# Kernel optimization log

Measured on AMD Instinct MI355X. Metric: run time of the kernel, lower is better.

The kernel has to match this reference:

```python
import jax, jax.numpy as jnp
import numpy as np

IO_EMB = 128; IO_HID = 512; ENC_HID = 1024
B = 256; N_IO = 4; L = 64; T = 32; NPROD = 64; VOCAB = 128


def setup_inputs() -> dict:
    key = jax.random.key(0)
    ks = jax.random.split(key, 16)
    s = 0.02
    return {
        'exs_toks': jax.random.randint(ks[0], (L, B * N_IO), 0, VOCAB),
        'cls_toks': jax.random.randint(ks[1], (L, B * N_IO), 0, VOCAB),
        'E_io': jax.random.normal(ks[2], (VOCAB, IO_EMB)) * s,
        'Wi_f': jax.random.normal(ks[3], (2 * IO_EMB, 4 * IO_HID)) * s,
        'Wh_f': jax.random.normal(ks[4], (IO_HID, 4 * IO_HID)) * s,
        'b_f': jnp.zeros((4 * IO_HID,)),
        'Wi_b': jax.random.normal(ks[5], (2 * IO_EMB, 4 * IO_HID)) * s,
        'Wh_b': jax.random.normal(ks[6], (IO_HID, 4 * IO_HID)) * s,
        'b_b': jnp.zeros((4 * IO_HID,)),
        'W_attn': jax.random.normal(ks[7], (ENC_HID, 2 * IO_HID)) * s,
        'W_comp': jax.random.normal(ks[8], (ENC_HID + 2 * IO_HID, NPROD)) * s,
        'b_comp': jnp.zeros((NPROD,)),
        'v_Wi': jax.random.normal(ks[9], (ENC_HID, 4 * ENC_HID)) * s,
        'v_Wh': jax.random.normal(ks[10], (ENC_HID, 4 * ENC_HID)) * s,
        'v_b': jnp.zeros((4 * ENC_HID,)),
        'field_emb': jax.random.normal(ks[11], (T, ENC_HID)) * s,
        'actions': jax.random.randint(ks[12], (B, T), 0, NPROD),
    }


def _lstm(x, Wi, Wh, b, reverse=False):
    # x: [L, N, D] -> hs [L, N, H], final (h, c)
    H = Wh.shape[0]
    N = x.shape[1]
    def step(carry, xt):
        h, c = carry
        g = xt @ Wi + h @ Wh + b
        i, f, gg, o = jnp.split(g, 4, axis=-1)
        c = jax.nn.sigmoid(f) * c + jax.nn.sigmoid(i) * jnp.tanh(gg)
        h = jax.nn.sigmoid(o) * jnp.tanh(c)
        return (h, c), h
    init = (jnp.zeros((N, H), x.dtype), jnp.zeros((N, H), x.dtype))
    (hT, cT), hs = jax.lax.scan(step, init, x, reverse=reverse)
    return hs, hT, cT


def reference(exs_toks, cls_toks, E_io, Wi_f, Wh_f, b_f, Wi_b, Wh_b, b_b,
              W_attn, W_comp, b_comp, v_Wi, v_Wh, v_b, field_emb, actions):
    # --- encode_io: concat exs/cls embeddings, run biLSTM ---
    x = jnp.concatenate([E_io[exs_toks], E_io[cls_toks]], axis=-1)  # [L, B*N_IO, 2*IO_EMB]
    hs_f, hTf, cTf = _lstm(x, Wi_f, Wh_f, b_f)
    hs_b, hTb, cTb = _lstm(x, Wi_b, Wh_b, b_b, reverse=True)
    ctx_vecs = jnp.concatenate([hs_f, hs_b], -1).reshape(L, B, N_IO, 2 * IO_HID)
    # init decoder state: max over io examples of final biLSTM state
    h0 = jnp.concatenate([hTf, hTb], -1).reshape(B, N_IO, ENC_HID).max(axis=1)
    c0 = jnp.concatenate([cTf, cTb], -1).reshape(B, N_IO, ENC_HID).max(axis=1)

    def dec_step(carry, xs):
        h, c, acc = carry
        x_t, a_t = xs  # field embedding [ENC_HID], action ids [B]
        # Luong attention over io context vecs, per io example, then max-pool
        q = h @ W_attn                               # [B, 2*IO_HID]
        scores = jnp.einsum('lbne,be->lbn', ctx_vecs, q)
        attn = jax.nn.softmax(scores, axis=0)
        ctx = jnp.einsum('lbn,lbne->bne', attn, ctx_vecs).max(axis=1)  # [B, 2*IO_HID]
        # per-node classifier (composite type module): negative log-prob of chosen prod
        logits = jnp.concatenate([h, ctx], -1) @ W_comp + b_comp
        logp = jax.nn.log_softmax(logits, axis=-1)
        acc = acc - logp[jnp.arange(B), a_t]
        # constructor update via v_lstm cell
        g = x_t @ v_Wi + h @ v_Wh + v_b
        i, f, gg, o = jnp.split(g, 4, axis=-1)
        c = jax.nn.sigmoid(f) * c + jax.nn.sigmoid(i) * jnp.tanh(gg)
        h = jax.nn.sigmoid(o) * jnp.tanh(c)
        return (h, c, acc), None

    init = (h0, c0, jnp.zeros((B,), h0.dtype))
    (_, _, total), _ = jax.lax.scan(dec_step, init, (field_emb, actions.T))
    return total  # [B] per-program negative log-likelihood
```

## Files before the change

### kernel.cpp

```cpp
#include <hip/hip_runtime.h>
#include <hip/hip_bf16.h>

typedef __bf16 bf16x8 __attribute__((ext_vector_type(8)));
typedef float  f32x4  __attribute__((ext_vector_type(4)));
typedef float  f32x2  __attribute__((ext_vector_type(2)));
typedef unsigned int u32x4 __attribute__((ext_vector_type(4)));
typedef unsigned short ushort_t;
static_assert(sizeof(bf16x8) == 16, "bf16x8 must be 16B");

#define DEV __device__ __forceinline__

DEV f32x4 mfma16(bf16x8 a, bf16x8 b, f32x4 c) {
    return __builtin_amdgcn_mfma_f32_16x16x32_bf16(a, b, c, 0, 0, 0);
}
DEV f32x4 mfma8(long a, long b, f32x4 c) {
    return __builtin_amdgcn_mfma_f32_16x16x32_fp8_fp8(a, b, c, 0, 0, 0);
}
DEV float sigm(float x)   { return 1.0f / (1.0f + __expf(-x)); }
DEV float tanh_f(float x) { return 2.0f / (1.0f + __expf(-2.0f * x)) - 1.0f; }

DEV void glds16(const __hip_bfloat16* g, __hip_bfloat16* l) {
    __builtin_amdgcn_global_load_lds(
        (const __attribute__((address_space(1))) unsigned int*)g,
        (__attribute__((address_space(3))) unsigned int*)l, 16, 0, 0);
}

DEV unsigned char f32_to_fp8(float v) {
    int p = __builtin_amdgcn_cvt_pk_fp8_f32(v, v, 0, false);
    return (unsigned char)(p & 0xFF);
}

DEV int i4get(const int4& v, int r) {
    return r == 0 ? v.x : r == 1 ? v.y : r == 2 ? v.z : v.w;
}

__global__ __launch_bounds__(128) void kdetect(const unsigned int* __restrict__ raw,
                                               int* __restrict__ mode) {
    __shared__ int cnt;
    if (threadIdx.x == 0) cnt = 0;
    __syncthreads();
    unsigned int w = raw[threadIdx.x];
    unsigned short lo = (unsigned short)(w & 0xFFFFu);
    unsigned int f32bits = ((unsigned int)lo) << 16;
    float v;
    __builtin_memcpy(&v, &f32bits, 4);
    float a = fabsf(v);
    if (a >= 1e-4f && a <= 1.0f) atomicAdd(&cnt, 1);
    __syncthreads();
    if (threadIdx.x == 0) *mode = (cnt >= 64) ? 1 : 0;
}

struct CvtArgs {
    const void* src[6];
    void* dst[6];
    int n[6];
    int bf16out[6];
};
__global__ __launch_bounds__(256) void kcvt_all(CvtArgs a, const int* __restrict__ mode) {
    int seg = blockIdx.y;
    int i = blockIdx.x * 256 + threadIdx.x;
    if (i >= a.n[seg]) return;
    int m = *mode;
    if (a.bf16out[seg]) {
        __hip_bfloat16* d = (__hip_bfloat16*)a.dst[seg];
        d[i] = m ? ((const __hip_bfloat16*)a.src[seg])[i]
                 : __float2bfloat16(((const float*)a.src[seg])[i]);
    } else {
        float* d = (float*)a.dst[seg];
        d[i] = m ? __bfloat162float(((const __hip_bfloat16*)a.src[seg])[i])
                 : ((const float*)a.src[seg])[i];
    }
}

struct TransArgs {
    const void* src[8];
    __hip_bfloat16* dst[8];
    int R[8];
    int C[8];
};
__global__ __launch_bounds__(256) void ktrans_all(TransArgs a, const int* __restrict__ mode) {
    __shared__ float tile[64][65];
    int id = blockIdx.z;
    int R = a.R[id], C = a.C[id];
    int c0 = blockIdx.x * 64, r0 = blockIdx.y * 64;
    if (c0 >= C || r0 >= R) return;
    const void* src = a.src[id];
    __hip_bfloat16* out = a.dst[id];
    int tx = threadIdx.x & 63, ty = threadIdx.x >> 6;
    int m = *mode;
#pragma unroll
    for (int i = ty; i < 64; i += 4) {
        size_t ix = (size_t)(r0 + i) * C + (c0 + tx);
        tile[i][tx] = m ? __bfloat162float(((const __hip_bfloat16*)src)[ix])
                        : ((const float*)src)[ix];
    }
    __syncthreads();
#pragma unroll
    for (int i = ty; i < 64; i += 4)
        out[(size_t)(c0 + i) * R + (r0 + tx)] = __float2bfloat16(tile[tx][i]);
}

__global__ __launch_bounds__(256) void kprep_all(
    const __hip_bfloat16* __restrict__ E,
    const __hip_bfloat16* __restrict__ WiT,
    const float* __restrict__ bF,
    const float* __restrict__ bB,
    float* __restrict__ G,
    const __hip_bfloat16* __restrict__ fe,
    const __hip_bfloat16* __restrict__ vWiT,
    const float* __restrict__ vb,
    float* __restrict__ VX)
{
    int lane = threadIdx.x & 63, wid = threadIdx.x >> 6;
    int r16 = lane & 15, quad = lane >> 4;

    if (blockIdx.x < 256) {
        int bid = blockIdx.x;
        int dh = bid >> 6;
        int dir = dh >> 1, half = dh & 1;
        int m0 = ((bid >> 5) & 1) * 64;
        int n0 = (bid & 31) * 64;
        int wrow = wid >> 1, wcol = wid & 1;

        f32x4 acc[2][2] = {};
        const __hip_bfloat16* Ap = E + (size_t)(m0 + wrow * 32 + r16) * 128 + quad * 8;
        const __hip_bfloat16* Bp = WiT + (size_t)dir * 2048 * 256
                                 + (size_t)(n0 + wcol * 32 + r16) * 256 + half * 128 + quad * 8;
#pragma unroll
        for (int kb = 0; kb < 128; kb += 32) {
            bf16x8 a0 = *(const bf16x8*)(Ap + kb);
            bf16x8 a1 = *(const bf16x8*)(Ap + 16 * 128 + kb);
            bf16x8 b0 = *(const bf16x8*)(Bp + kb);
            bf16x8 b1 = *(const bf16x8*)(Bp + 16 * 256 + kb);
            acc[0][0] = mfma16(a0, b0, acc[0][0]);
            acc[0][1] = mfma16(a0, b1, acc[0][1]);
            acc[1][0] = mfma16(a1, b0, acc[1][0]);
            acc[1][1] = mfma16(a1, b1, acc[1][1]);
        }
        const float* bias = dir ? bB : bF;
        float* Gt = G + (size_t)dh * 128 * 2048;
#pragma unroll
        for (int rt = 0; rt < 2; rt++)
#pragma unroll
            for (int ct = 0; ct < 2; ct++)
#pragma unroll
                for (int r = 0; r < 4; r++) {
                    int mm = m0 + wrow * 32 + rt * 16 + quad * 4 + r;
                    int j = n0 + wcol * 32 + ct * 16 + r16;
                    float v = acc[rt][ct][r];
                    if (half == 0) v += bias[j];
                    int g = j >> 9, u = j & 511;
                    Gt[((size_t)mm * 512 + u) * 4 + g] = v;
                }
    } else {
        int n0 = (blockIdx.x - 256) * 128;
        f32x4 acc[2][2] = {};
        const __hip_bfloat16* Ap = fe + (size_t)r16 * 1024 + quad * 8;
        const __hip_bfloat16* Bp = vWiT + (size_t)(n0 + wid * 32 + r16) * 1024 + quad * 8;
        for (int kb = 0; kb < 1024; kb += 32) {
            bf16x8 a0 = *(const bf16x8*)(Ap + kb);
            bf16x8 a1 = *(const bf16x8*)(Ap + 16 * 1024 + kb);
            bf16x8 b0 = *(const bf16x8*)(Bp + kb);
            bf16x8 b1 = *(const bf16x8*)(Bp + 16 * 1024 + kb);
            acc[0][0] = mfma16(a0, b0, acc[0][0]);
            acc[0][1] = mfma16(a0, b1, acc[0][1]);
            acc[1][0] = mfma16(a1, b0, acc[1][0]);
            acc[1][1] = mfma16(a1, b1, acc[1][1]);
        }
#pragma unroll
        for (int rt = 0; rt < 2; rt++)
#pragma unroll
            for (int ct = 0; ct < 2; ct++)
#pragma unroll
                for (int r = 0; r < 4; r++) {
                    int m = rt * 16 + quad * 4 + r;
                    int j = n0 + wid * 32 + ct * 16 + r16;
                    VX[(size_t)m * 4096 + j] = acc[rt][ct][r] + vb[j];
                }
    }
}

__global__ __launch_bounds__(256, 2) void kenc_step(
    int t,
    const __hip_bfloat16* __restrict__ WhT,
    const float* __restrict__ Gtab,
    const int* __restrict__ exs,
    const int* __restrict__ cls,
    const __hip_bfloat16* __restrict__ h_in,
    __hip_bfloat16* __restrict__ h_out,
    float* __restrict__ c_st,
    unsigned char* __restrict__ ctx8)
{
    __shared__ __align__(16) __hip_bfloat16 sA[3][64 * 64];
    __shared__ __align__(16) __hip_bfloat16 sB[3][128 * 64];

    int bid = blockIdx.x;
    int dir = bid >> 8;
    int mt  = (bid >> 4) & 15;
    int us  = bid & 15;
    int l = dir ? (63 - t) : t;
    int m0 = mt * 64, u0 = us * 32;

    int lane = threadIdx.x & 63, w = threadIdx.x >> 6;
    int wm = w >> 1, wu = w & 1;
    int r16 = lane & 15, quad = lane >> 4;
    int srow = lane >> 3;
    int scol = ((lane & 7) ^ srow) * 8;

    const __hip_bfloat16* Ab = h_in + (size_t)dir * 1024 * 512;
    const __hip_bfloat16* Bb = WhT + (size_t)dir * 2048 * 512;

    int u = u0 + wu * 16 + r16;
    int mbase = m0 + wm * 32;
    size_t cbase = (size_t)dir * 1024 * 512;
    const float* GeT = Gtab + (size_t)(dir * 2) * 128 * 2048;
    const float* GcT = GeT + 128 * 2048;

    int4 tE0 = *(const int4*)&exs[l * 1024 + mbase + quad * 4];
    int4 tE1 = *(const int4*)&exs[l * 1024 + mbase + 16 + quad * 4];
    int4 tC0 = *(const int4*)&cls[l * 1024 + mbase + quad * 4];
    int4 tC1 = *(const int4*)&cls[l * 1024 + mbase + 16 + quad * 4];

    f32x4 acc[4][2] = {};
    f32x4 geP[2][4], gcP[2][4];
    float cP[2][4];

    auto stage = [&](int buf, int it) {
        int kb = it * 64;
#pragma unroll
        for (int c = 0; c < 2; c++) {
            int r8 = (w * 2 + c) * 8;
            glds16(Ab + (size_t)(m0 + r8 + srow) * 512 + kb + scol,
                   &sA[buf][r8 * 64]);
        }
#pragma unroll
        for (int c = 0; c < 4; c++) {
            int rl = (w * 4 + c) * 8;
            int rr = rl + srow;
            int g = rr >> 5, j = rr & 31;
            glds16(Bb + (size_t)(g * 512 + u0 + j) * 512 + kb + scol,
                   &sB[buf][rl * 64]);
        }
    };

    stage(0, 0);
    stage(1, 1);

    const int sw = r16 & 7;
    const int NIT = 8;
#pragma unroll
    for (int it = 0; it < NIT; it++) {
        if (it < NIT - 1)
            asm volatile("s_waitcnt vmcnt(6) lgkmcnt(0)" ::: "memory");
        else
            asm volatile("s_waitcnt vmcnt(24) lgkmcnt(0)" ::: "memory");
        __builtin_amdgcn_s_barrier();
        if (it + 2 < NIT) {
            stage((it + 2) % 3, it + 2);
        } else if (it == NIT - 2) {
#pragma unroll
            for (int mi = 0; mi < 2; mi++)
#pragma unroll
                for (int r = 0; r < 4; r++) {
                    int vE = i4get(mi ? tE1 : tE0, r);
                    int vC = i4get(mi ? tC1 : tC0, r);
                    geP[mi][r] = *(const f32x4*)&GeT[((size_t)vE * 512 + u) * 4];
                    gcP[mi][r] = *(const f32x4*)&GcT[((size_t)vC * 512 + u) * 4];
                    int m = mbase + mi * 16 + quad * 4 + r;
                    cP[mi][r] = c_st[cbase + (size_t)m * 512 + u];
                }
        }
        const int buf = it % 3;
#pragma unroll
        for (int k32 = 0; k32 < 64; k32 += 32) {
            int co = (((k32 >> 3) + quad) ^ sw) * 8;
            bf16x8 a[2], bf[4];
#pragma unroll
            for (int mi = 0; mi < 2; mi++)
                a[mi] = *(const bf16x8*)&sA[buf][(wm * 32 + mi * 16 + r16) * 64 + co];
#pragma unroll
            for (int g = 0; g < 4; g++)
                bf[g] = *(const bf16x8*)&sB[buf][(g * 32 + wu * 16 + r16) * 64 + co];
#pragma unroll
            for (int g = 0; g < 4; g++)
#pragma unroll
                for (int mi = 0; mi < 2; mi++)
                    acc[g][mi] = mfma16(a[mi], bf[g], acc[g][mi]);
        }
    }

#pragma unroll
    for (int mi = 0; mi < 2; mi++)
#pragma unroll
        for (int r = 0; r < 4; r++) {
            int m = mbase + mi * 16 + quad * 4 + r;
            f32x4 ge = geP[mi][r];
            f32x4 gc = gcP[mi][r];
            float gi = acc[0][mi][r] + ge[0] + gc[0];
            float gf = acc[1][mi][r] + ge[1] + gc[1];
            float gg = acc[2][mi][r] + ge[2] + gc[2];
            float go = acc[3][mi][r] + ge[3] + gc[3];
            size_t cix = cbase + (size_t)m * 512 + u;
            float cn = sigm(gf) * cP[mi][r] + sigm(gi) * tanh_f(gg);
            c_st[cix] = cn;
            float hn = sigm(go) * tanh_f(cn);
            h_out[cix] = __float2bfloat16(hn);
            ctx8[(((size_t)l * 256 + (m >> 2)) * 4 + (m & 3)) * 1024 + dir * 512 + u]
                = f32_to_fp8(hn * 16.0f);
        }
}

__global__ __launch_bounds__(256) void ktrans8_init(
    const unsigned char* __restrict__ ctx8,
    unsigned char* __restrict__ ctxT8,
    const __hip_bfloat16* __restrict__ hf,
    const float* __restrict__ cf,
    __hip_bfloat16* __restrict__ h0,
    float* __restrict__ c0)
{
    __shared__ unsigned int tile[64][17];
    int bx = blockIdx.x;
    int tid = threadIdx.x;
    if (bx < 16384) {
        int b4n = bx & 1023;
        int e0 = (bx >> 10) * 64;
#pragma unroll
        for (int pass = 0; pass < 4; pass++) {
            int idx = pass * 256 + tid;
            int l = idx >> 4, c = idx & 15;
            tile[l][c] = *(const unsigned int*)(ctx8 + (size_t)l * (1024 * 1024)
                                                + (size_t)b4n * 1024 + e0 + c * 4);
        }
        __syncthreads();
        const unsigned char* tb = (const unsigned char*)tile;
#pragma unroll
        for (int pass = 0; pass < 4; pass++) {
            int idx = pass * 256 + tid;
            int e = idx >> 4, c = idx & 15;
            unsigned int v = 0;
#pragma unroll
            for (int j = 0; j < 4; j++) {
                unsigned int byte = tb[(size_t)(c * 4 + j) * 68 + e];
                v |= byte << (8 * j);
            }
            *(unsigned int*)(ctxT8 + ((size_t)b4n * 1024 + e0 + e) * 64 + c * 4) = v;
        }
    } else {
        int idx = (bx - 16384) * 256 + tid;
        int b = idx >> 10, e = idx & 1023;
        int dir = e >> 9, u = e & 511;
        const __hip_bfloat16* hs = hf + (size_t)dir * 1024 * 512;
        const float* cs = cf + (size_t)dir * 1024 * 512;
        float hv = -3.4e38f, cv = -3.4e38f;
#pragma unroll
        for (int n = 0; n < 4; n++) {
            size_t ix = (size_t)(b * 4 + n) * 512 + u;
            hv = fmaxf(hv, __bfloat162float(hs[ix]));
            cv = fmaxf(cv, cs[ix]);
        }
        h0[idx] = __float2bfloat16(hv);
        c0[idx] = cv;
    }
}

__global__ __launch_bounds__(256, 2) void kdec_gemm(
    int t,
    const __hip_bfloat16* __restrict__ vWhT,
    const __hip_bfloat16* __restrict__ WattnT,
    const float* __restrict__ VX,
    const __hip_bfloat16* __restrict__ h_in,
    __hip_bfloat16* __restrict__ h_out,
    float* __restrict__ c_st,
    float* __restrict__ qout)
{
    __shared__ __align__(16) __hip_bfloat16 sA[3][64 * 64];
    __shared__ __align__(16) __hip_bfloat16 sB[3][128 * 64];

    int bid = blockIdx.x;
    int lane = threadIdx.x & 63, w = threadIdx.x >> 6;
    int wm = w >> 1, wu = w & 1;
    int r16 = lane & 15, quad = lane >> 4;
    int srow = lane >> 3;
    int scol = ((lane & 7) ^ srow) * 8;
    const int NIT = 16;
    const int sw = r16 & 7;

    bool cellp = bid < 128;
    int b2 = cellp ? bid : bid - 128;
    int m0 = (b2 >> 5) * 64;
    int n0 = (b2 & 31) * 32;
    int u = n0 + wu * 16 + r16;
    int mbase = m0 + wm * 32;

    if (cellp) {
        f32x4 acc[4][2] = {};
        float vxP[4], cP[2][4];
        const float* vx = VX + (size_t)t * 4096;
        auto stage = [&](int buf, int it) {
            int kb = it * 64;
#pragma unroll
            for (int c = 0; c < 2; c++) {
                int r8 = (w * 2 + c) * 8;
                glds16(h_in + (size_t)(m0 + r8 + srow) * 1024 + kb + scol,
                       &sA[buf][r8 * 64]);
            }
#pragma unroll
            for (int c = 0; c < 4; c++) {
                int rl = (w * 4 + c) * 8;
                int rr = rl + srow;
                int g = rr >> 5, j = rr & 31;
                glds16(vWhT + (size_t)(g * 1024 + n0 + j) * 1024 + kb + scol,
                       &sB[buf][rl * 64]);
            }
        };
        stage(0, 0);
        stage(1, 1);
#pragma unroll
        for (int it = 0; it < NIT; it++) {
            if (it < NIT - 1)
                asm volatile("s_waitcnt vmcnt(6) lgkmcnt(0)" ::: "memory");
            else
                asm volatile("s_waitcnt vmcnt(12) lgkmcnt(0)" ::: "memory");
            __builtin_amdgcn_s_barrier();
            if (it + 2 < NIT) {
                stage((it + 2) % 3, it + 2);
            } else if (it == NIT - 2) {
                vxP[0] = vx[u];
                vxP[1] = vx[1024 + u];
                vxP[2] = vx[2048 + u];
                vxP[3] = vx[3072 + u];
#pragma unroll
                for (int mi = 0; mi < 2; mi++)
#pragma unroll
                    for (int r = 0; r < 4; r++) {
                        int m = mbase + mi * 16 + quad * 4 + r;
                        cP[mi][r] = c_st[(size_t)m * 1024 + u];
                    }
            }
            const int buf = it % 3;
#pragma unroll
            for (int k32 = 0; k32 < 64; k32 += 32) {
                int co = (((k32 >> 3) + quad) ^ sw) * 8;
                bf16x8 a[2], bf[4];
#pragma unroll
                for (int mi = 0; mi < 2; mi++)
                    a[mi] = *(const bf16x8*)&sA[buf][(wm * 32 + mi * 16 + r16) * 64 + co];
#pragma unroll
                for (int g = 0; g < 4; g++)
                    bf[g] = *(const bf16x8*)&sB[buf][(g * 32 + wu * 16 + r16) * 64 + co];
#pragma unroll
                for (int g = 0; g < 4; g++)
#pragma unroll
                    for (int mi = 0; mi < 2; mi++)
                        acc[g][mi] = mfma16(a[mi], bf[g], acc[g][mi]);
            }
        }
#pragma unroll
        for (int mi = 0; mi < 2; mi++)
#pragma unroll
            for (int r = 0; r < 4; r++) {
                int m = mbase + mi * 16 + quad * 4 + r;
                float gi = acc[0][mi][r] + vxP[0];
                float gf = acc[1][mi][r] + vxP[1];
                float gg = acc[2][mi][r] + vxP[2];
                float go = acc[3][mi][r] + vxP[3];
                size_t cix = (size_t)m * 1024 + u;
                float cn = sigm(gf) * cP[mi][r] + sigm(gi) * tanh_f(gg);
                c_st[cix] = cn;
                h_out[cix] = __float2bfloat16(sigm(go) * tanh_f(cn));
            }
    } else {
        f32x4 acc[2] = {};
        auto stage = [&](int buf, int it) {
            int kb = it * 64;
#pragma unroll
            for (int c = 0; c < 2; c++) {
                int r8 = (w * 2 + c) * 8;
                glds16(h_in + (size_t)(m0 + r8 + srow) * 1024 + kb + scol,
                       &sA[buf][r8 * 64]);
            }
            {
                int rl = w * 8;
                glds16(WattnT + (size_t)(n0 + rl + srow) * 1024 + kb + scol,
                       &sB[buf][rl * 64]);
            }
        };
        stage(0, 0);
        stage(1, 1);
#pragma unroll
        for (int it = 0; it < NIT; it++) {
            if (it < NIT - 1)
                asm volatile("s_waitcnt vmcnt(3) lgkmcnt(0)" ::: "memory");
            else
                asm volatile("s_waitcnt vmcnt(0) lgkmcnt(0)" ::: "memory");
            __builtin_amdgcn_s_barrier();
            if (it + 2 < NIT) stage((it + 2) % 3, it + 2);
            const int buf = it % 3;
#pragma unroll
            for (int k32 = 0; k32 < 64; k32 += 32) {
                int co = (((k32 >> 3) + quad) ^ sw) * 8;
                bf16x8 a[2];
#pragma unroll
                for (int mi = 0; mi < 2; mi++)
                    a[mi] = *(const bf16x8*)&sA[buf][(wm * 32 + mi * 16 + r16) * 64 + co];
                bf16x8 bf = *(const bf16x8*)&sB[buf][(wu * 16 + r16) * 64 + co];
#pragma unroll
                for (int mi = 0; mi < 2; mi++)
                    acc[mi] = mfma16(a[mi], bf, acc[mi]);
            }
        }
        int n = n0 + wu * 16 + r16;
#pragma unroll
        for (int mi = 0; mi < 2; mi++)
#pragma unroll
            for (int r = 0; r < 4; r++) {
                int m = mbase + mi * 16 + quad * 4 + r;
                qout[(size_t)m * 1024 + n] = acc[mi][r];
            }
    }
}

__global__ __launch_bounds__(512, 2) void kattn_mfma(
    const float* __restrict__ qall,
    const unsigned char* __restrict__ ctx8,
    const unsigned char* __restrict__ ctxT8,
    const __hip_bfloat16* __restrict__ hAll,
    const __hip_bfloat16* __restrict__ WcT,
    const float* __restrict__ bcomp,
    const int* __restrict__ actions,
    float* __restrict__ nllT)
{
    __shared__ __align__(16) char smem[75520];
    unsigned char* sQ8   = (unsigned char*)smem;
    float*         sS    = (float*)(smem + 33024);
    unsigned char* sP    = (unsigned char*)(smem + 66304);
    ushort_t*      sPool = (ushort_t*)smem;
    float*         slg   = (float*)(smem + 66304);

    int b = blockIdx.x;
    int tid = threadIdx.x;
    int lane = tid & 63, w = tid >> 6;
    int r16 = lane & 15, quad = lane >> 4;
    const size_t LSTR = 1024 * 1024;

    for (int i = 0; i < 64; i++) {
        int idx = i * 512 + tid;
        int t = idx >> 10, e = idx & 1023;
        float v = qall[((size_t)t * 256 + b) * 1024 + e] * 0.25f;
        sQ8[t * 1032 + e] = f32_to_fp8(v);
    }
    __syncthreads();

    {
        int n = w >> 1, lh = w & 1;
        int l0 = lh * 32;
        f32x4 c[2][2] = {};
        const unsigned char* cbase = ctx8 + (size_t)(b * 4 + n) * 1024;
        for (int k0 = 0; k0 < 1024; k0 += 32) {
            long a[2], bv[2];
#pragma unroll
            for (int mt = 0; mt < 2; mt++)
                __builtin_memcpy(&a[mt], &sQ8[(mt * 16 + r16) * 1032 + k0 + quad * 8], 8);
#pragma unroll
            for (int lt = 0; lt < 2; lt++)
                bv[lt] = *(const long*)(cbase + (size_t)(l0 + lt * 16 + r16) * LSTR
                                        + k0 + quad * 8);
#pragma unroll
            for (int mt = 0; mt < 2; mt++)
#pragma unroll
                for (int lt = 0; lt < 2; lt++)
                    c[mt][lt] = mfma8(a[mt], bv[lt], c[mt][lt]);
        }
#pragma unroll
        for (int mt = 0; mt < 2; mt++)
#pragma unroll
            for (int lt = 0; lt < 2; lt++)
#pragma unroll
                for (int r = 0; r < 4; r++)
                    sS[(n * 32 + mt * 16 + quad * 4 + r) * 65 + l0 + lt * 16 + r16]
                        = c[mt][lt][r];
    }
    __syncthreads();

    if (tid < 128) {
        int n = tid >> 5, t = tid & 31;
        const float* row = &sS[(n * 32 + t) * 65];
        float sum = 0.f;
        for (int l = 0; l < 64; l++)
            sum += __expf(fminf(row[l] * 0.25f, 60.f));
        float inv = 16.0f / sum;
        unsigned char* pr = &sP[(n * 32 + t) * 72];
        for (int l = 0; l < 64; l++)
            pr[l] = f32_to_fp8(__expf(fminf(row[l] * 0.25f, 60.f)) * inv);
    }
    __syncthreads();

    {
        int e0 = w * 128;
        f32x4 pool[2][8];
#pragma unroll
        for (int mt = 0; mt < 2; mt++)
#pragma unroll
            for (int et = 0; et < 8; et++)
#pragma unroll
                for (int r = 0; r < 4; r++) pool[mt][et][r] = -3.4e38f;

        for (int n = 0; n < 4; n++) {
            f32x4 c[2][8] = {};
            const unsigned char* tbase = ctxT8 + (size_t)(b * 4 + n) * 1024 * 64;
#pragma unroll
            for (int k0 = 0; k0 < 64; k0 += 32) {
                long a[2];
#pragma unroll
                for (int mt = 0; mt < 2; mt++)
                    __builtin_memcpy(&a[mt], &sP[(n * 32 + mt * 16 + r16) * 72 + k0 + quad * 8], 8);
#pragma unroll
                for (int et = 0; et < 8; et++) {
                    long bv = *(const long*)(tbase + (size_t)(e0 + et * 16 + r16) * 64
                                             + k0 + quad * 8);
#pragma unroll
                    for (int mt = 0; mt < 2; mt++)
                        c[mt][et] = mfma8(a[mt], bv, c[mt][et]);
                }
            }
#pragma unroll
            for (int mt = 0; mt < 2; mt++)
#pragma unroll
                for (int et = 0; et < 8; et++)
#pragma unroll
                    for (int r = 0; r < 4; r++)
                        pool[mt][et][r] = fmaxf(pool[mt][et][r], c[mt][et][r] * (1.0f / 256.0f));
        }
        __syncthreads();
#pragma unroll
        for (int mt = 0; mt < 2; mt++)
#pragma unroll
            for (int et = 0; et < 8; et++)
#pragma unroll
                for (int r = 0; r < 4; r++) {
                    int t = mt * 16 + quad * 4 + r;
                    int e = e0 + et * 16 + r16;
                    __hip_bfloat16 hb = __float2bfloat16(pool[mt][et][r]);
                    sPool[t * 1032 + e] = *(ushort_t*)&hb;
                }
    }
    __syncthreads();

    {
        int mt = w & 1, pt = w >> 1;
        f32x4 c = {};
        const __hip_bfloat16* hrow = hAll + ((size_t)(mt * 16 + r16) * 256 + b) * 1024;
        const __hip_bfloat16* wrow = WcT + (size_t)(pt * 16 + r16) * 2048;
        for (int k0 = 0; k0 < 2048; k0 += 32) {
            bf16x8 a;
            if (k0 < 1024)
                a = *(const bf16x8*)(hrow + k0 + quad * 8);
            else
                a = *(const bf16x8*)&sPool[(mt * 16 + r16) * 1032 + (k0 - 1024) + quad * 8];
            bf16x8 bv = *(const bf16x8*)(wrow + k0 + quad * 8);
            c = mfma16(a, bv, c);
        }
        __syncthreads();
#pragma unroll
        for (int r = 0; r < 4; r++) {
            int t = mt * 16 + quad * 4 + r;
            int p = pt * 16 + r16;
            slg[t * 68 + p] = c[r] + bcomp[p];
        }
    }
    __syncthreads();

    if (tid < 32) {
        int t = tid;
        const float* row = &slg[t * 68];
        float m = -3.4e38f;
        for (int p = 0; p < 64; p++) m = fmaxf(m, row[p]);
        float se = 0.f;
        for (int p = 0; p < 64; p++) se += __expf(row[p] - m);
        int a = actions[b * 32 + t];
        nllT[t * 256 + b] = m + __logf(se) - row[a];
    }
}

__global__ void kfinal(const float* __restrict__ nllT, void* __restrict__ out,
                       const int* __restrict__ mode) {
    int i = threadIdx.x;
    float s = 0.f;
#pragma unroll
    for (int t = 0; t < 32; t++) s += nllT[t * 256 + i];
    if (*mode) ((__hip_bfloat16*)out)[i] = __float2bfloat16(s);
    else       ((float*)out)[i] = s;
}

extern "C" void kernel_launch(void* const* d_in, const int* in_sizes, int n_in,
                              void* d_out, int out_size, void* d_ws, size_t ws_size,
                              hipStream_t stream) {
    const int* exs = (const int*)d_in[0];
    const int* cls = (const int*)d_in[1];
    const void* E_raw     = d_in[2];
    const void* WiF_raw   = d_in[3];
    const void* WhF_raw   = d_in[4];
    const void* bF_raw    = d_in[5];
    const void* WiB_raw   = d_in[6];
    const void* WhB_raw   = d_in[7];
    const void* bB_raw    = d_in[8];
    const void* Wattn_raw = d_in[9];
    const void* Wcomp_raw = d_in[10];
    const void* bcomp_raw = d_in[11];
    const void* vWi_raw   = d_in[12];
    const void* vWh_raw   = d_in[13];
    const void* vb_raw    = d_in[14];
    const void* fe_raw    = d_in[15];
    const int* actions = (const int*)d_in[16];
    (void)in_sizes; (void)n_in; (void)out_size; (void)ws_size;

    char* w = (char*)d_ws;
    size_t off = 0;
    auto take = [&](size_t bytes) -> char* {
        char* p = w + off;
        off = (off + bytes + 255) & ~(size_t)255;
        return p;
    };
    __hip_bfloat16* WhT    = (__hip_bfloat16*)take(2ull * 2048 * 512 * 2);
    __hip_bfloat16* WiT    = (__hip_bfloat16*)take(2ull * 2048 * 256 * 2);
    __hip_bfloat16* vWhT   = (__hip_bfloat16*)take(4096ull * 1024 * 2);
    __hip_bfloat16* vWiT   = (__hip_bfloat16*)take(4096ull * 1024 * 2);
    __hip_bfloat16* WattnT = (__hip_bfloat16*)take(1024ull * 1024 * 2);
    __hip_bfloat16* WcT    = (__hip_bfloat16*)take(64ull * 2048 * 2);
    __hip_bfloat16* Ebf    = (__hip_bfloat16*)take(128ull * 128 * 2);
    __hip_bfloat16* febf   = (__hip_bfloat16*)take(32ull * 1024 * 2);
    float* bFf   = (float*)take(2048 * 4);
    float* bBf   = (float*)take(2048 * 4);
    float* bcf   = (float*)take(64 * 4);
    float* vbf   = (float*)take(4096 * 4);
    float* Gtab  = (float*)take(4ull * 128 * 2048 * 4);
    float* VX    = (float*)take(32ull * 4096 * 4);
    __hip_bfloat16* hEnc = (__hip_bfloat16*)take(2ull * 2 * 1024 * 512 * 2);
    float* cEnc = (float*)take(2ull * 1024 * 512 * 4);
    __hip_bfloat16* hAll = (__hip_bfloat16*)take(33ull * 256 * 1024 * 2);
    float* cDec = (float*)take(256ull * 1024 * 4);
    float* qall = (float*)take(32ull * 256 * 1024 * 4);
    float* nllT = (float*)take(32ull * 256 * 4);
    int*   mode = (int*)take(256);
    unsigned char* ctx8  = (unsigned char*)take(64ull * 1024 * 1024);
    unsigned char* ctxT8 = (unsigned char*)take(64ull * 1024 * 1024);

    (void)hipMemsetAsync(hEnc, 0, 2ull * 1024 * 512 * 2, stream);
    (void)hipMemsetAsync(cEnc, 0, 2ull * 1024 * 512 * 4, stream);

    kdetect<<<1, 128, 0, stream>>>((const unsigned int*)E_raw, mode);

    {
        CvtArgs ca;
        ca.src[0] = E_raw;     ca.dst[0] = Ebf;  ca.n[0] = 128 * 128;  ca.bf16out[0] = 1;
        ca.src[1] = fe_raw;    ca.dst[1] = febf; ca.n[1] = 32 * 1024;  ca.bf16out[1] = 1;
        ca.src[2] = bF_raw;    ca.dst[2] = bFf;  ca.n[2] = 2048;       ca.bf16out[2] = 0;
        ca.src[3] = bB_raw;    ca.dst[3] = bBf;  ca.n[3] = 2048;       ca.bf16out[3] = 0;
        ca.src[4] = bcomp_raw; ca.dst[4] = bcf;  ca.n[4] = 64;         ca.bf16out[4] = 0;
        ca.src[5] = vb_raw;    ca.dst[5] = vbf;  ca.n[5] = 4096;       ca.bf16out[5] = 0;
        kcvt_all<<<dim3(128, 6), 256, 0, stream>>>(ca, mode);
    }

    {
        TransArgs ta;
        ta.src[0] = WhF_raw;   ta.dst[0] = WhT;              ta.R[0] = 512;  ta.C[0] = 2048;
        ta.src[1] = WhB_raw;   ta.dst[1] = WhT + 2048 * 512; ta.R[1] = 512;  ta.C[1] = 2048;
        ta.src[2] = WiF_raw;   ta.dst[2] = WiT;              ta.R[2] = 256;  ta.C[2] = 2048;
        ta.src[3] = WiB_raw;   ta.dst[3] = WiT + 2048 * 256; ta.R[3] = 256;  ta.C[3] = 2048;
        ta.src[4] = vWh_raw;   ta.dst[4] = vWhT;             ta.R[4] = 1024; ta.C[4] = 4096;
        ta.src[5] = vWi_raw;   ta.dst[5] = vWiT;             ta.R[5] = 1024; ta.C[5] = 4096;
        ta.src[6] = Wattn_raw; ta.dst[6] = WattnT;           ta.R[6] = 1024; ta.C[6] = 1024;
        ta.src[7] = Wcomp_raw; ta.dst[7] = WcT;              ta.R[7] = 2048; ta.C[7] = 64;
        ktrans_all<<<dim3(64, 32, 8), 256, 0, stream>>>(ta, mode);
    }

    kprep_all<<<288, 256, 0, stream>>>(Ebf, WiT, bFf, bBf, Gtab, febf, vWiT, vbf, VX);

    const size_t HB = 2ull * 1024 * 512;
    for (int t = 0; t < 64; t++) {
        kenc_step<<<512, 256, 0, stream>>>(t, WhT, Gtab, exs, cls,
                                           hEnc + (size_t)(t & 1) * HB,
                                           hEnc + (size_t)((t + 1) & 1) * HB,
                                           cEnc, ctx8);
    }
    ktrans8_init<<<16384 + 1024, 256, 0, stream>>>(ctx8, ctxT8, hEnc, cEnc, hAll, cDec);

    const size_t HD = 256ull * 1024;
    for (int t = 0; t < 32; t++) {
        kdec_gemm<<<256, 256, 0, stream>>>(t, vWhT, WattnT, VX,
                                           hAll + (size_t)t * HD,
                                           hAll + (size_t)(t + 1) * HD,
                                           cDec, qall + (size_t)t * HD);
    }
    kattn_mfma<<<256, 512, 0, stream>>>(qall, ctx8, ctxT8, hAll, WcT, bcf,
                                        actions, nllT);
    kfinal<<<1, 256, 0, stream>>>(nllT, d_out, mode);
}
```

Before: 1.457 ms.

## Split attention kernel across two time halves per batch and split-K classifier

The attention/classifier kernel now runs 512 blocks, each handling 16 decoder timesteps for one batch item, instead of 256 blocks covering all 32. This halves shared memory per block and fills more CUs. The classifier GEMM is split along K between warp pairs, one doing the hidden-state half and one the pooled-context half, with partial logits summed in the final softmax. The trade-off is that each block re-reads the context tensors (ctx8, ctxT8) for its batch item, doubling that global traffic.

Result: no change. 1.484 ms (+1.9%).

```diff
diff --git a/kernel.cpp b/kernel.cpp
--- a/kernel.cpp
+++ b/kernel.cpp
@@ -530,66 +530,59 @@
     const int* __restrict__ actions,
     float* __restrict__ nllT)
 {
-    __shared__ __align__(16) char smem[75520];
+    __shared__ __align__(16) char smem[41856];
     unsigned char* sQ8   = (unsigned char*)smem;
-    float*         sS    = (float*)(smem + 33024);
-    unsigned char* sP    = (unsigned char*)(smem + 66304);
+    float*         sS    = (float*)(smem + 16512);
+    unsigned char* sP    = (unsigned char*)(smem + 33152);
     ushort_t*      sPool = (ushort_t*)smem;
-    float*         slg   = (float*)(smem + 66304);
-
-    int b = blockIdx.x;
+    float*         slg2  = (float*)(smem + 33152);
+
+    int bb = blockIdx.x;
+    int b = bb >> 1, t0 = (bb & 1) * 16;
     int tid = threadIdx.x;
     int lane = tid & 63, w = tid >> 6;
     int r16 = lane & 15, quad = lane >> 4;
     const size_t LSTR = 1024 * 1024;
 
-    for (int i = 0; i < 64; i++) {
+    for (int i = 0; i < 32; i++) {
         int idx = i * 512 + tid;
-        int t = idx >> 10, e = idx & 1023;
-        float v = qall[((size_t)t * 256 + b) * 1024 + e] * 0.25f;
-        sQ8[t * 1032 + e] = f32_to_fp8(v);
+        int tl = idx >> 10, e = idx & 1023;
+        float v = qall[((size_t)(t0 + tl) * 256 + b) * 1024 + e] * 0.25f;
+        sQ8[tl * 1032 + e] = f32_to_fp8(v);
     }
     __syncthreads();
 
     {
         int n = w >> 1, lh = w & 1;
         int l0 = lh * 32;
-        f32x4 c[2][2] = {};
+        f32x4 c[2] = {};
         const unsigned char* cbase = ctx8 + (size_t)(b * 4 + n) * 1024;
         for (int k0 = 0; k0 < 1024; k0 += 32) {
-            long a[2], bv[2];
-#pragma unroll
-            for (int mt = 0; mt < 2; mt++)
-                __builtin_memcpy(&a[mt], &sQ8[(mt * 16 + r16) * 1032 + k0 + quad * 8], 8);
-#pragma unroll
-            for (int lt = 0; lt < 2; lt++)
-                bv[lt] = *(const long*)(cbase + (size_t)(l0 + lt * 16 + r16) * LSTR
-                                        + k0 + quad * 8);
-#pragma unroll
-            for (int mt = 0; mt < 2; mt++)
-#pragma unroll
-                for (int lt = 0; lt < 2; lt++)
-                    c[mt][lt] = mfma8(a[mt], bv[lt], c[mt][lt]);
-        }
-#pragma unroll
-        for (int mt = 0; mt < 2; mt++)
-#pragma unroll
-            for (int lt = 0; lt < 2; lt++)
-#pragma unroll
-                for (int r = 0; r < 4; r++)
-                    sS[(n * 32 + mt * 16 + quad * 4 + r) * 65 + l0 + lt * 16 + r16]
-                        = c[mt][lt][r];
+            long a;
+            __builtin_memcpy(&a, &sQ8[r16 * 1032 + k0 + quad * 8], 8);
+#pragma unroll
+            for (int lt = 0; lt < 2; lt++) {
+                long bv = *(const long*)(cbase + (size_t)(l0 + lt * 16 + r16) * LSTR
+                                         + k0 + quad * 8);
+                c[lt] = mfma8(a, bv, c[lt]);
+            }
+        }
+#pragma unroll
+        for (int lt = 0; lt < 2; lt++)
+#pragma unroll
+            for (int r = 0; r < 4; r++)
+                sS[(n * 16 + quad * 4 + r) * 65 + l0 + lt * 16 + r16] = c[lt][r];
     }
     __syncthreads();
 
-    if (tid < 128) {
-        int n = tid >> 5, t = tid & 31;
-        const float* row = &sS[(n * 32 + t) * 65];
+    if (tid < 64) {
+        int n = tid >> 4, tl = tid & 15;
+        const float* row = &sS[(n * 16 + tl) * 65];
         float sum = 0.f;
         for (int l = 0; l < 64; l++)
             sum += __expf(fminf(row[l] * 0.25f, 60.f));
         float inv = 16.0f / sum;
-        unsigned char* pr = &sP[(n * 32 + t) * 72];
+        unsigned char* pr = &sP[(n * 16 + tl) * 72];
         for (int l = 0; l < 64; l++)
             pr[l] = f32_to_fp8(__expf(fminf(row[l] * 0.25f, 60.f)) * inv);
     }
@@ -597,88 +590,82 @@
 
     {
         int e0 = w * 128;
-        f32x4 pool[2][8];
-#pragma unroll
-        for (int mt = 0; mt < 2; mt++)
-#pragma unroll
-            for (int et = 0; et < 8; et++)
-#pragma unroll
-                for (int r = 0; r < 4; r++) pool[mt][et][r] = -3.4e38f;
+        f32x4 pool[8];
+#pragma unroll
+        for (int et = 0; et < 8; et++)
+#pragma unroll
+            for (int r = 0; r < 4; r++) pool[et][r] = -3.4e38f;
 
         for (int n = 0; n < 4; n++) {
-            f32x4 c[2][8] = {};
+            f32x4 c[8] = {};
             const unsigned char* tbase = ctxT8 + (size_t)(b * 4 + n) * 1024 * 64;
 #pragma unroll
             for (int k0 = 0; k0 < 64; k0 += 32) {
-                long a[2];
-#pragma unroll
-                for (int mt = 0; mt < 2; mt++)
-                    __builtin_memcpy(&a[mt], &sP[(n * 32 + mt * 16 + r16) * 72 + k0 + quad * 8], 8);
+                long a;
+                __builtin_memcpy(&a, &sP[(n * 16 + r16) * 72 + k0 + quad * 8], 8);
 #pragma unroll
                 for (int et = 0; et < 8; et++) {
                     long bv = *(const long*)(tbase + (size_t)(e0 + et * 16 + r16) * 64
                                              + k0 + quad * 8);
-#pragma unroll
-                    for (int mt = 0; mt < 2; mt++)
-                        c[mt][et] = mfma8(a[mt], bv, c[mt][et]);
+                    c[et] = mfma8(a, bv, c[et]);
                 }
             }
 #pragma unroll
-            for (int mt = 0; mt < 2; mt++)
-#pragma unroll
-                for (int et = 0; et < 8; et++)
-#pragma unroll
-                    for (int r = 0; r < 4; r++)
-                        pool[mt][et][r] = fmaxf(pool[mt][et][r], c[mt][et][r] * (1.0f / 256.0f));
+            for (int et = 0; et < 8; et++)
+#pragma unroll
+                for (int r = 0; r < 4; r++)
+                    pool[et][r] = fmaxf(pool[et][r], c[et][r] * (1.0f / 256.0f));
+        }
+#pragma unroll
+        for (int et = 0; et < 8; et++)
+#pragma unroll
+            for (int r = 0; r < 4; r++) {
+                int tl = quad * 4 + r;
+                int e = e0 + et * 16 + r16;
+                __hip_bfloat16 hb = __float2bfloat16(pool[et][r]);
+                sPool[tl * 1032 + e] = *(ushort_t*)&hb;
+            }
+    }
+    __syncthreads();
+
+    {
+        int pt = w >> 1, kh = w & 1;
+        f32x4 c = {};
+        const __hip_bfloat16* wrow = WcT + (size_t)(pt * 16 + r16) * 2048 + kh * 1024;
+        if (kh == 0) {
+            const __hip_bfloat16* hrow = hAll + ((size_t)(t0 + r16) * 256 + b) * 1024;
+            for (int k0 = 0; k0 < 1024; k0 += 32) {
+                bf16x8 a = *(const bf16x8*)(hrow + k0 + quad * 8);
+                bf16x8 bv = *(const bf16x8*)(wrow + k0 + quad * 8);
+                c = mfma16(a, bv, c);
+            }
+        } else {
+            for (int k0 = 0; k0 < 1024; k0 += 32) {
+                bf16x8 a = *(const bf16x8*)&sPool[r16 * 1032 + k0 + quad * 8];
+                bf16x8 bv = *(const bf16x8*)(wrow + k0 + quad * 8);
+                c = mfma16(a, bv, c);
+            }
         }
         __syncthreads();
 #pragma unroll
-        for (int mt = 0; mt < 2; mt++)
-#pragma unroll
-            for (int et = 0; et < 8; et++)
-#pragma unroll
-                for (int r = 0; r < 4; r++) {
-                    int t = mt * 16 + quad * 4 + r;
-                    int e = e0 + et * 16 + r16;
-                    __hip_bfloat16 hb = __float2bfloat16(pool[mt][et][r]);
-                    sPool[t * 1032 + e] = *(ushort_t*)&hb;
-                }
+        for (int r = 0; r < 4; r++) {
+            int tl = quad * 4 + r;
+            int p = pt * 16 + r16;
+            slg2[(kh * 16 + tl) * 68 + p] = c[r] + (kh ? 0.f : bcomp[p]);
+        }
     }
     __syncthreads();
 
-    {
-        int mt = w & 1, pt = w >> 1;
-        f32x4 c = {};
-        const __hip_bfloat16* hrow = hAll + ((size_t)(mt * 16 + r16) * 256 + b) * 1024;
-        const __hip_bfloat16* wrow = WcT + (size_t)(pt * 16 + r16) * 2048;
-        for (int k0 = 0; k0 < 2048; k0 += 32) {
-            bf16x8 a;
-            if (k0 < 1024)
-                a = *(const bf16x8*)(hrow + k0 + quad * 8);
-            else
-                a = *(const bf16x8*)&sPool[(mt * 16 + r16) * 1032 + (k0 - 1024) + quad * 8];
-            bf16x8 bv = *(const bf16x8*)(wrow + k0 + quad * 8);
-            c = mfma16(a, bv, c);
-        }
-        __syncthreads();
-#pragma unroll
-        for (int r = 0; r < 4; r++) {
-            int t = mt * 16 + quad * 4 + r;
-            int p = pt * 16 + r16;
-            slg[t * 68 + p] = c[r] + bcomp[p];
-        }
-    }
-    __syncthreads();
-
-    if (tid < 32) {
-        int t = tid;
-        const float* row = &slg[t * 68];
+    if (tid < 16) {
+        int tl = tid;
+        const float* r0 = &slg2[tl * 68];
+        const float* r1 = &slg2[(16 + tl) * 68];
         float m = -3.4e38f;
-        for (int p = 0; p < 64; p++) m = fmaxf(m, row[p]);
+        for (int p = 0; p < 64; p++) m = fmaxf(m, r0[p] + r1[p]);
         float se = 0.f;
-        for (int p = 0; p < 64; p++) se += __expf(row[p] - m);
-        int a = actions[b * 32 + t];
-        nllT[t * 256 + b] = m + __logf(se) - row[a];
+        for (int p = 0; p < 64; p++) se += __expf(r0[p] + r1[p] - m);
+        int a = actions[b * 32 + t0 + tl];
+        nllT[(size_t)(t0 + tl) * 256 + b] = m + __logf(se) - (r0[a] + r1[a]);
     }
 }
 
@@ -792,7 +779,7 @@
                                            hAll + (size_t)(t + 1) * HD,
                                            cDec, qall + (size_t)t * HD);
     }
-    kattn_mfma<<<256, 512, 0, stream>>>(qall, ctx8, ctxT8, hAll, WcT, bcf,
+    kattn_mfma<<<512, 512, 0, stream>>>(qall, ctx8, ctxT8, hAll, WcT, bcf,
                                         actions, nllT);
     kfinal<<<1, 256, 0, stream>>>(nllT, d_out, mode);
 }
```
